# Kernel tuning notes

Measured on AMD Instinct MI355X. Metric: run time of the kernel, lower is better.

## Reference

```python
import jax, jax.numpy as jnp
import numpy as np

L, B, T, C, H, V = 12, 4, 1024, 768, 12, 50257
D = C // H
SCALE = 1.0 / float(np.sqrt(D))
EPS = 1e-5


def layernorm(x, g, b):
    m = jnp.mean(x, axis=-1, keepdims=True)
    v = jnp.var(x, axis=-1, keepdims=True)
    return (x - m) / jnp.sqrt(v + EPS) * g + b


def setup_inputs() -> dict:
    key = jax.random.key(0)
    ks = jax.random.split(key, 12)
    w = lambda k, shape: jax.random.normal(k, shape, jnp.float32) * 0.02
    return {
        "idx": jax.random.randint(ks[0], (B, T), 0, V),
        "tok_emb": w(ks[1], (V, C)),
        "pos_emb": w(ks[2], (1, T, C)),
        # per-layer stacked params (leading dim L); Linear stored [in, out]
        "wq": w(ks[3], (L, C, C)), "bq": jnp.zeros((L, C)),
        "wk": w(ks[4], (L, C, C)), "bk": jnp.zeros((L, C)),
        "wv": w(ks[5], (L, C, C)), "bv": jnp.zeros((L, C)),
        "wo": w(ks[6], (L, C, C)), "bo": jnp.zeros((L, C)),
        "ln1_g": jnp.ones((L, C)), "ln1_b": jnp.zeros((L, C)),
        "ln2_g": jnp.ones((L, C)), "ln2_b": jnp.zeros((L, C)),
        "w1": w(ks[7], (L, C, 4 * C)), "b1": jnp.zeros((L, 4 * C)),
        "w2": w(ks[8], (L, 4 * C, C)), "b2": jnp.zeros((L, C)),
        "lnf_g": jnp.ones((C,)), "lnf_b": jnp.zeros((C,)),
        "head_w": w(ks[9], (C, V)),
    }


def gpt_forward(idx, tok_emb, pos_emb, wq, bq, wk, bk, wv, bv, wo, bo,
                ln1_g, ln1_b, ln2_g, ln2_b, w1, b1, w2, b2,
                lnf_g, lnf_b, head_w):
    t = idx.shape[1]
    x = tok_emb[idx] + pos_emb[:, :t, :]                     # [B,T,C]
    mask = jnp.tril(jnp.ones((t, t), dtype=bool))            # causal

    def block(x, p):
        (pwq, pbq, pwk, pbk, pwv, pbv, pwo, pbo,
         g1, be1, g2, be2, pw1, pb1, pw2, pb2) = p
        h = layernorm(x, g1, be1)
        q = (h @ pwq + pbq).reshape(B, t, H, D)
        k = (h @ pwk + pbk).reshape(B, t, H, D)
        v = (h @ pwv + pbv).reshape(B, t, H, D)
        att = jnp.einsum('bthd,bshd->bhts', q, k) * SCALE    # [B,H,T,T]
        att = jnp.where(mask, att, -jnp.inf)
        att = jax.nn.softmax(att, axis=-1)
        y = jnp.einsum('bhts,bshd->bthd', att, v).reshape(B, t, C)
        x = x + y @ pwo + pbo
        h = layernorm(x, g2, be2)
        x = x + jax.nn.gelu(h @ pw1 + pb1, approximate=False) @ pw2 + pb2
        return x, None

    x, _ = jax.lax.scan(block, x, (wq, bq, wk, bk, wv, bv, wo, bo,
                                   ln1_g, ln1_b, ln2_g, ln2_b,
                                   w1, b1, w2, b2))
    x = layernorm(x, lnf_g, lnf_b)
    return x @ head_w                                        # logits [B,T,V]


def reference(idx, tok_emb, pos_emb, wq, bq, wk, bk, wv, bv, wo, bo,
              ln1_g, ln1_b, ln2_g, ln2_b, w1, b1, w2, b2,
              lnf_g, lnf_b, head_w):
    return gpt_forward(idx, tok_emb, pos_emb, wq, bq, wk, bk, wv, bv, wo, bo,
                       ln1_g, ln1_b, ln2_g, ln2_b, w1, b1, w2, b2,
                       lnf_g, lnf_b, head_w)
```

## Files before the change

kernel.cpp:

```cpp
#include <hip/hip_runtime.h>
#include <hip/hip_bf16.h>
#include <math.h>

#define L_ 12
#define B_ 4
#define T_ 1024
#define C_ 768
#define H_ 12
#define D_ 64
#define V_ 50257
#define M_ 4096
#define QKVN 2304
#define FF_ 3072
#define VPAD_ 51200

typedef __hip_bfloat16 bf16;
typedef __attribute__((ext_vector_type(4))) float f32x4;
typedef __attribute__((ext_vector_type(4))) short short4v;
typedef __attribute__((ext_vector_type(8))) short short8;
typedef __attribute__((ext_vector_type(8))) __bf16 bf16x8;

typedef __attribute__((address_space(1))) void gvoid;
typedef __attribute__((address_space(3))) void svoid;

__device__ __forceinline__ f32x4 mfma_bf16(short8 a, short8 b, f32x4 c) {
  return __builtin_amdgcn_mfma_f32_16x16x32_bf16(
      __builtin_bit_cast(bf16x8, a), __builtin_bit_cast(bf16x8, b), c, 0, 0, 0);
}

__device__ __forceinline__ void gload_lds16(const void* g, void* l) {
  __builtin_amdgcn_global_load_lds((gvoid*)(void*)g, (svoid*)l, 16, 0, 0);
}

__device__ __forceinline__ short f2bf(float x) {
  return __builtin_bit_cast(short, __float2bfloat16(x));
}

__global__ __launch_bounds__(256) void embed_kernel(const int* __restrict__ idx,
    const float* __restrict__ tok, const float* __restrict__ pos, float* __restrict__ x)
{
  const int row = blockIdx.x;
  const int t = row & (T_ - 1);
  const int id = idx[row];
  const float* te = tok + (size_t)id * C_;
  const float* pe = pos + (size_t)t * C_;
  float* xr = x + (size_t)row * C_;
  const int tid = threadIdx.x;
  xr[tid]       = te[tid]       + pe[tid];
  xr[tid + 256] = te[tid + 256] + pe[tid + 256];
  xr[tid + 512] = te[tid + 512] + pe[tid + 512];
}

__global__ __launch_bounds__(256) void ln_kernel(const float* __restrict__ x,
    const float* __restrict__ g, const float* __restrict__ be, bf16* __restrict__ out)
{
  const int w = threadIdx.x >> 6, l = threadIdx.x & 63;
  const int row = blockIdx.x * 4 + w;
  const float* xr = x + (size_t)row * C_;
  f32x4 v[3];
  float s = 0.0f, ss = 0.0f;
#pragma unroll
  for (int p = 0; p < 3; p++) {
    v[p] = *(const f32x4*)&xr[p * 256 + l * 4];
#pragma unroll
    for (int e = 0; e < 4; e++) { s += v[p][e]; ss += v[p][e] * v[p][e]; }
  }
#pragma unroll
  for (int o = 32; o >= 1; o >>= 1) { s += __shfl_xor(s, o, 64); ss += __shfl_xor(ss, o, 64); }
  const float mean = s * (1.0f / C_);
  const float rstd = rsqrtf(ss * (1.0f / C_) - mean * mean + 1e-5f);
  bf16* orow = out + (size_t)row * C_;
#pragma unroll
  for (int p = 0; p < 3; p++) {
    const f32x4 gg = *(const f32x4*)&g[p * 256 + l * 4];
    const f32x4 bb = *(const f32x4*)&be[p * 256 + l * 4];
    short4v o4;
#pragma unroll
    for (int e = 0; e < 4; e++) o4[e] = f2bf((v[p][e] - mean) * rstd * gg[e] + bb[e]);
    *(short4v*)&orow[p * 256 + l * 4] = o4;
  }
}

__global__ __launch_bounds__(256) void convt_kernel(const float* __restrict__ in,
    bf16* __restrict__ out, int K, int N, long in_ls, long out_ls, int row_off)
{
  __shared__ float tile[64][65];
  in  += (size_t)blockIdx.z * in_ls;
  out += (size_t)blockIdx.z * out_ls;
  const int k0 = blockIdx.x * 64, n0 = blockIdx.y * 64;
  const int tid = threadIdx.x;
#pragma unroll
  for (int ph = 0; ph < 4; ph++) {
    const int lk = ph * 16 + (tid >> 4);
    const int ln = (tid & 15) * 4;
    const int gn = n0 + ln;
    const float* src = &in[(size_t)(k0 + lk) * N + gn];
    f32x4 vv;
    if (gn + 4 <= N) {
      vv = *(const f32x4*)src;
    } else {
#pragma unroll
      for (int e = 0; e < 4; e++) vv[e] = (gn + e < N) ? src[e] : 0.0f;
    }
    *(f32x4*)&tile[lk][ln] = vv;
  }
  __syncthreads();
#pragma unroll
  for (int ph = 0; ph < 2; ph++) {
    const int lon = ph * 32 + (tid >> 3);
    const int lok0 = (tid & 7) * 8;
    short8 o;
#pragma unroll
    for (int e = 0; e < 8; e++) o[e] = f2bf(tile[lok0 + e][lon]);
    *(short8*)&out[(size_t)(row_off + n0 + lon) * K + k0 + lok0] = o;
  }
}

__global__ __launch_bounds__(256) void packb_kernel(const float* __restrict__ bq,
    const float* __restrict__ bk, const float* __restrict__ bv, float* __restrict__ out)
{
  const int i = blockIdx.x * 256 + threadIdx.x;
  const int ly = i / QKVN, c = i % QKVN;
  float v;
  if (c < C_)            v = bq[ly * C_ + c];
  else if (c < 2 * C_)   v = bk[ly * C_ + c - C_];
  else                   v = bv[ly * C_ + c - 2 * C_];
  out[i] = v;
}

template<bool BIAS, bool GELU, bool RESID, bool BF16OUT, bool VT>
__global__ __launch_bounds__(256) void gemm_bt(
    const short* __restrict__ A, const short* __restrict__ Bt,
    const float* __restrict__ bias, const float* resid,
    void* out, short* __restrict__ vt, int M, int N, int K)
{
  __shared__ short As[128 * 64];
  __shared__ short Bs[128 * 64];
  const int tid = threadIdx.x;
  const int w = tid >> 6, l = tid & 63;
  const int l15 = l & 15, l4 = l >> 4;
  const int wr = w >> 1, wc = w & 1;
  const int nwg = gridDim.x * gridDim.y;
  const int id = blockIdx.y * gridDim.x + blockIdx.x;
  const int chunk = nwg >> 3;
  const int swz = (id & 7) * chunk + (id >> 3);
  const long m0 = (long)(swz % gridDim.x) * 128;
  const long n0 = (long)(swz / gridDim.x) * 128;

  f32x4 acc[4][4] = {};
  const int lrow8 = l >> 3;
  const int lc = l & 7;

  for (int kt = 0; kt < K; kt += 64) {
#pragma unroll
    for (int j = 0; j < 8; j++) {
      const int c = w * 8 + j;
      const int isA = (c < 16);
      const int cc = isA ? c : (c - 16);
      const int row = cc * 8 + lrow8;
      const int colsw = ((lc ^ (row & 7)) << 3);
      const short* gp = (isA ? A + (size_t)(m0 + row) * K : Bt + (size_t)(n0 + row) * K) + kt + colsw;
      short* sp = (isA ? As : Bs) + row * 64 + (lc << 3);
      gload_lds16(gp, sp);
    }
    __syncthreads();
#pragma unroll
    for (int ks = 0; ks < 2; ks++) {
      short8 af[4], bfr[4];
#pragma unroll
      for (int i = 0; i < 4; i++) {
        int row = wr * 64 + i * 16 + l15;
        int cs = (ks * 32 + l4 * 8) ^ ((row & 7) << 3);
        af[i] = *(const short8*)&As[row * 64 + cs];
      }
#pragma unroll
      for (int jn = 0; jn < 4; jn++) {
        int row = wc * 64 + jn * 16 + l15;
        int cs = (ks * 32 + l4 * 8) ^ ((row & 7) << 3);
        bfr[jn] = *(const short8*)&Bs[row * 64 + cs];
      }
#pragma unroll
      for (int i = 0; i < 4; i++)
#pragma unroll
        for (int jn = 0; jn < 4; jn++)
          acc[i][jn] = mfma_bf16(af[i], bfr[jn], acc[i][jn]);
    }
    __syncthreads();
  }

#pragma unroll
  for (int i = 0; i < 4; i++) {
    const long rbase = m0 + wr * 64 + i * 16 + l4 * 4;
#pragma unroll
    for (int jn = 0; jn < 4; jn++) {
      const long col = n0 + wc * 64 + jn * 16 + l15;
      const float bv = BIAS ? bias[col] : 0.0f;
      if (VT && col >= 2 * C_) {
        const int hd = (int)col - 2 * C_;
        const int b = (int)(rbase >> 10);
        const int t0 = (int)(rbase & 1023);
        short4v o4;
#pragma unroll
        for (int r = 0; r < 4; r++) o4[r] = f2bf(acc[i][jn][r] + bv);
        *(short4v*)&vt[((size_t)(b * H_) * D_ + hd) * T_ + t0] = o4;
      } else {
#pragma unroll
        for (int r = 0; r < 4; r++) {
          float v = acc[i][jn][r] + bv;
          if (GELU) v = 0.5f * v * (1.0f + erff(v * 0.70710678118654752f));
          const size_t o = (size_t)(rbase + r) * (size_t)N + col;
          if (RESID)        ((float*)out)[o] = resid[o] + v;
          else if (BF16OUT) ((bf16*)out)[o] = __float2bfloat16(v);
          else              ((float*)out)[o] = v;
        }
      }
    }
  }
}

template<bool BIAS, bool GELU, bool RESID, bool BF16OUT>
__global__ __launch_bounds__(256) void gemm64(
    const short* __restrict__ A, const short* __restrict__ Bt,
    const float* __restrict__ bias, const float* resid,
    void* out, int M, int N, int K)
{
  __shared__ short As[64 * 64];
  __shared__ short Bs[128 * 64];
  const int tid = threadIdx.x;
  const int w = tid >> 6, l = tid & 63;
  const int l15 = l & 15, l4 = l >> 4;
  const int wm = w >> 1, wn = w & 1;
  const int nwg = gridDim.x * gridDim.y;
  const int id = blockIdx.y * gridDim.x + blockIdx.x;
  const int chunk = nwg >> 3;
  const int swz = (id & 7) * chunk + (id >> 3);
  const long m0 = (long)(swz % gridDim.x) * 64;
  const long n0 = (long)(swz / gridDim.x) * 128;
  const int rr = tid >> 3, g = tid & 7;

  f32x4 acc[2][4] = {};

  for (int kt = 0; kt < K; kt += 64) {
#pragma unroll
    for (int p = 0; p < 2; p++) {
      const int row = p * 32 + rr;
      const int cg = ((g ^ (row & 7)) << 3);
      gload_lds16(A + (size_t)(m0 + row) * K + kt + cg, &As[row * 64 + g * 8]);
    }
#pragma unroll
    for (int p = 0; p < 4; p++) {
      const int row = p * 32 + rr;
      const int cg = ((g ^ (row & 7)) << 3);
      gload_lds16(Bt + (size_t)(n0 + row) * K + kt + cg, &Bs[row * 64 + g * 8]);
    }
    __syncthreads();
#pragma unroll
    for (int ks = 0; ks < 2; ks++) {
      short8 af[2], bfr[4];
#pragma unroll
      for (int i = 0; i < 2; i++) {
        int row = wm * 32 + i * 16 + l15;
        int cs = (ks * 32 + l4 * 8) ^ ((row & 7) << 3);
        af[i] = *(const short8*)&As[row * 64 + cs];
      }
#pragma unroll
      for (int j = 0; j < 4; j++) {
        int row = wn * 64 + j * 16 + l15;
        int cs = (ks * 32 + l4 * 8) ^ ((row & 7) << 3);
        bfr[j] = *(const short8*)&Bs[row * 64 + cs];
      }
#pragma unroll
      for (int i = 0; i < 2; i++)
#pragma unroll
        for (int j = 0; j < 4; j++)
          acc[i][j] = mfma_bf16(af[i], bfr[j], acc[i][j]);
    }
    __syncthreads();
  }

#pragma unroll
  for (int i = 0; i < 2; i++) {
    const long rbase = m0 + wm * 32 + i * 16 + l4 * 4;
#pragma unroll
    for (int j = 0; j < 4; j++) {
      const long col = n0 + wn * 64 + j * 16 + l15;
      const float bv = BIAS ? bias[col] : 0.0f;
#pragma unroll
      for (int r = 0; r < 4; r++) {
        float v = acc[i][j][r] + bv;
        if (GELU) v = 0.5f * v * (1.0f + erff(v * 0.70710678118654752f));
        const size_t o = (size_t)(rbase + r) * (size_t)N + col;
        if (RESID)        ((float*)out)[o] = resid[o] + v;
        else if (BF16OUT) ((bf16*)out)[o] = __float2bfloat16(v);
        else              ((float*)out)[o] = v;
      }
    }
  }
}

__global__ __launch_bounds__(512, 1) void gemm256(
    const short* __restrict__ A, const short* __restrict__ Bt,
    float* __restrict__ out, int N, int K)
{
  __shared__ short As[2][256 * 64];
  __shared__ short Bs[2][256 * 64];
  const int tid = threadIdx.x;
  const int l = tid & 63, l15 = l & 15, l4 = l >> 4;
  const int wv = tid >> 6, wm = wv >> 2, wn = wv & 3;
  const int bid = blockIdx.x;
  const int x = bid & 7, r = bid >> 3;
  const int mt = (x & 1) * 8 + (r & 7);
  const int nt = (x >> 1) * 50 + (r >> 3);
  const long m0 = (long)mt * 256;
  const long n0 = (long)nt * 256;
  const int nkt = K >> 6;
  const int rr = tid >> 3, g = tid & 7;

  f32x4 acc[8][4] = {};

  auto stA = [&](int s, int kt, int off) {
#pragma unroll
    for (int p = 0; p < 2; p++) {
      const int row = p * 128 + off + rr;
      gload_lds16(A + (size_t)(m0 + row) * K + (kt << 6) + ((g ^ (row & 7)) << 3),
                  &As[s][row * 64 + g * 8]);
    }
  };
  auto stB = [&](int s, int kt, int off) {
#pragma unroll
    for (int p = 0; p < 2; p++) {
      const int row = p * 128 + ((rr >> 5) << 6) + (rr & 31) + off;
      gload_lds16(Bt + (size_t)(n0 + row) * K + (kt << 6) + ((g ^ (row & 7)) << 3),
                  &Bs[s][row * 64 + g * 8]);
    }
  };
  auto rdA = [&](int s, int mf, int ks) {
    const int row = wm * 128 + mf * 16 + l15;
    const int cs = (ks * 32 + l4 * 8) ^ ((row & 7) << 3);
    return *(const short8*)&As[s][row * 64 + cs];
  };
  auto rdB = [&](int s, int nf, int ks) {
    const int row = wn * 64 + nf * 16 + l15;
    const int cs = (ks * 32 + l4 * 8) ^ ((row & 7) << 3);
    return *(const short8*)&Bs[s][row * 64 + cs];
  };

  stA(0, 0, 0); stB(0, 0, 0); stA(0, 0, 64); stB(0, 0, 32);

  int q = 0;
  for (int kt = 0; kt < nkt; ++kt, q ^= 1) {
    const int ktn = (kt + 1 < nkt) ? kt + 1 : kt;
    short8 a0[2][4], a1[2][4], b0[2][2], b1[2][2];

    stA(q ^ 1, ktn, 0);
    asm volatile("s_waitcnt vmcnt(6)" ::: "memory");
    __builtin_amdgcn_s_barrier();
#pragma unroll
    for (int ks = 0; ks < 2; ks++) {
#pragma unroll
      for (int f = 0; f < 4; f++) a0[ks][f] = rdA(q, f, ks);
#pragma unroll
      for (int j = 0; j < 2; j++) b0[ks][j] = rdB(q, j, ks);
    }
    __builtin_amdgcn_s_setprio(1);
#pragma unroll
    for (int f = 0; f < 4; f++)
#pragma unroll
      for (int j = 0; j < 2; j++) {
        acc[f][j] = mfma_bf16(a0[0][f], b0[0][j], acc[f][j]);
        acc[f][j] = mfma_bf16(a0[1][f], b0[1][j], acc[f][j]);
      }
    __builtin_amdgcn_s_setprio(0);

    stB(q ^ 1, ktn, 0);
    asm volatile("s_waitcnt vmcnt(6)" ::: "memory");
    __builtin_amdgcn_s_barrier();
#pragma unroll
    for (int ks = 0; ks < 2; ks++)
#pragma unroll
      for (int f = 0; f < 4; f++) a1[ks][f] = rdA(q, f + 4, ks);
    __builtin_amdgcn_s_setprio(1);
#pragma unroll
    for (int f = 0; f < 4; f++)
#pragma unroll
      for (int j = 0; j < 2; j++) {
        acc[f + 4][j] = mfma_bf16(a1[0][f], b0[0][j], acc[f + 4][j]);
        acc[f + 4][j] = mfma_bf16(a1[1][f], b0[1][j], acc[f + 4][j]);
      }
    __builtin_amdgcn_s_setprio(0);

    stA(q ^ 1, ktn, 64);
    asm volatile("s_waitcnt vmcnt(6)" ::: "memory");
    __builtin_amdgcn_s_barrier();
#pragma unroll
    for (int ks = 0; ks < 2; ks++)
#pragma unroll
      for (int j = 0; j < 2; j++) b1[ks][j] = rdB(q, j + 2, ks);
    __builtin_amdgcn_s_setprio(1);
#pragma unroll
    for (int f = 0; f < 4; f++)
#pragma unroll
      for (int j = 0; j < 2; j++) {
        acc[f][j + 2] = mfma_bf16(a0[0][f], b1[0][j], acc[f][j + 2]);
        acc[f][j + 2] = mfma_bf16(a0[1][f], b1[1][j], acc[f][j + 2]);
      }
    __builtin_amdgcn_s_setprio(0);

    stB(q ^ 1, ktn, 32);
    __builtin_amdgcn_s_setprio(1);
#pragma unroll
    for (int f = 0; f < 4; f++)
#pragma unroll
      for (int j = 0; j < 2; j++) {
        acc[f + 4][j + 2] = mfma_bf16(a1[0][f], b1[0][j], acc[f + 4][j + 2]);
        acc[f + 4][j + 2] = mfma_bf16(a1[1][f], b1[1][j], acc[f + 4][j + 2]);
      }
    __builtin_amdgcn_s_setprio(0);
  }

#pragma unroll
  for (int i = 0; i < 8; i++) {
#pragma unroll
    for (int j = 0; j < 4; j++) {
      const long col = n0 + wn * 64 + j * 16 + l15;
      if (col >= N) continue;
#pragma unroll
      for (int r2 = 0; r2 < 4; r2++) {
        const long row = m0 + wm * 128 + i * 16 + l4 * 4 + r2;
        out[(size_t)row * (size_t)N + col] = acc[i][j][r2];
      }
    }
  }
}

__global__ __launch_bounds__(256) void attn_kernel(const short* __restrict__ qkv,
    const short* __restrict__ vt, bf16* __restrict__ y)
{
  __shared__ short Ks[2][64 * 64];
  __shared__ short Vs[2][64 * 64];
  const int qt = (gridDim.x - 1) - blockIdx.x;
  const int bh = blockIdx.y;
  const int b = bh / H_, h = bh % H_;
  const int tid = threadIdx.x, w = tid >> 6, l = tid & 63;
  const int l15 = l & 15, l4 = l >> 4;
  const int qrow0 = qt * 64 + w * 16;
  const float SC2 = 0.125f * 1.44269504088896f;

  auto stageKV = [&](int s, int s0) {
    const short* kbase = qkv + (size_t)(b * T_ + s0) * QKVN + C_ + h * D_;
    const short* vsrc = vt + (size_t)bh * D_ * T_ + s0;
#pragma unroll
    for (int ph = 0; ph < 2; ph++) {
      int r = ph * 32 + (tid >> 3);
      int gk = ((tid & 7) ^ ((r & 3) | (((r >> 3) & 1) << 2))) << 3;
      int gv = ((tid & 7) ^ (r & 7)) << 3;
      gload_lds16(kbase + (size_t)r * QKVN + gk, &Ks[s][r * 64 + (tid & 7) * 8]);
      gload_lds16(vsrc + (size_t)r * T_ + gv, &Vs[s][r * 64 + (tid & 7) * 8]);
    }
  };

  short8 qf[2];
#pragma unroll
  for (int kf = 0; kf < 2; kf++)
    qf[kf] = *(const short8*)&qkv[(size_t)(b * T_ + qrow0 + l15) * QKVN + h * D_ + kf * 32 + l4 * 8];

  f32x4 O[4] = {};
  float mst = -1e30f, lst = 0.0f;

  stageKV(0, 0);
  __syncthreads();

  int cur = 0;
  const int qg = qrow0 + l15;
  const int send = qt * 64 + 64;
  for (int s0 = 0; s0 < send; s0 += 64) {
    if (s0 + 64 < send) stageKV(cur ^ 1, s0 + 64);
    f32x4 S[4];
#pragma unroll
    for (int c = 0; c < 4; c++) {
      const int row = 8 * (l15 >> 2) + (l15 & 3) + 4 * (c & 1) + 32 * (c >> 1);
      const int swz = (row & 3) | (((row >> 3) & 1) << 2);
      short8 k0 = *(const short8*)&Ks[cur][row * 64 + ((l4 ^ swz) << 3)];
      short8 k1 = *(const short8*)&Ks[cur][row * 64 + (((4 + l4) ^ swz) << 3)];
      f32x4 z = {0.0f, 0.0f, 0.0f, 0.0f};
      z = mfma_bf16(k0, qf[0], z);
      z = mfma_bf16(k1, qf[1], z);
      S[c] = z;
    }
#pragma unroll
    for (int c = 0; c < 4; c++) {
      const int kvb = s0 + 8 * l4 + 4 * (c & 1) + 32 * (c >> 1);
#pragma unroll
      for (int r = 0; r < 4; r++) {
        const float v = S[c][r] * SC2;
        S[c][r] = (kvb + r <= qg) ? v : -1e30f;
      }
    }
    float pm = -1e30f;
#pragma unroll
    for (int c = 0; c < 4; c++)
#pragma unroll
      for (int r = 0; r < 4; r++) pm = fmaxf(pm, S[c][r]);
    float mn;
    if (__all(pm - mst <= 8.0f)) {
      mn = mst;
    } else {
      float pm2 = fmaxf(pm, __shfl_xor(pm, 16, 64));
      pm2 = fmaxf(pm2, __shfl_xor(pm2, 32, 64));
      mn = fmaxf(mst, pm2);
      const float al = exp2f(mst - mn);
      mst = mn;
      lst *= al;
#pragma unroll
      for (int r = 0; r < 4; r++) {
        const float alr = __shfl(al, l4 * 4 + r, 16);
#pragma unroll
        for (int df = 0; df < 4; df++) O[df][r] *= alr;
      }
    }
    float rs = 0.0f;
    float pvv[4][4];
#pragma unroll
    for (int c = 0; c < 4; c++)
#pragma unroll
      for (int r = 0; r < 4; r++) { pvv[c][r] = exp2f(S[c][r] - mn); rs += pvv[c][r]; }
    rs += __shfl_xor(rs, 16, 64);
    rs += __shfl_xor(rs, 32, 64);
    lst += rs;
    short8 pa[2];
#pragma unroll
    for (int ks = 0; ks < 2; ks++)
#pragma unroll
      for (int r = 0; r < 4; r++) {
        pa[ks][r]     = f2bf(pvv[2 * ks][r]);
        pa[ks][r + 4] = f2bf(pvv[2 * ks + 1][r]);
      }
#pragma unroll
    for (int df = 0; df < 4; df++) {
      const int row = df * 16 + l15;
      short8 v0 = *(const short8*)&Vs[cur][row * 64 + ((l4 ^ (row & 7)) << 3)];
      short8 v1 = *(const short8*)&Vs[cur][row * 64 + ((((4 + l4)) ^ (row & 7)) << 3)];
      O[df] = mfma_bf16(pa[0], v0, O[df]);
      O[df] = mfma_bf16(pa[1], v1, O[df]);
    }
    __syncthreads();
    cur ^= 1;
  }

  const float inv = 1.0f / lst;
#pragma unroll
  for (int r = 0; r < 4; r++) {
    const float invr = __shfl(inv, l4 * 4 + r, 16);
    const size_t row = (size_t)(b * T_ + qrow0 + l4 * 4 + r);
#pragma unroll
    for (int df = 0; df < 4; df++)
      y[row * C_ + h * D_ + df * 16 + l15] = __float2bfloat16(O[df][r] * invr);
  }
}

extern "C" void kernel_launch(void* const* d_in, const int* in_sizes, int n_in,
                              void* d_out, int out_size, void* d_ws, size_t ws_size,
                              hipStream_t stream)
{
  const int*   idx  = (const int*)d_in[0];
  const float* tok  = (const float*)d_in[1];
  const float* pos  = (const float*)d_in[2];
  const float* wq   = (const float*)d_in[3];
  const float* bq   = (const float*)d_in[4];
  const float* wk   = (const float*)d_in[5];
  const float* bk   = (const float*)d_in[6];
  const float* wv   = (const float*)d_in[7];
  const float* bv   = (const float*)d_in[8];
  const float* wo   = (const float*)d_in[9];
  const float* bo   = (const float*)d_in[10];
  const float* ln1g = (const float*)d_in[11];
  const float* ln1b = (const float*)d_in[12];
  const float* ln2g = (const float*)d_in[13];
  const float* ln2b = (const float*)d_in[14];
  const float* w1   = (const float*)d_in[15];
  const float* b1   = (const float*)d_in[16];
  const float* w2   = (const float*)d_in[17];
  const float* b2   = (const float*)d_in[18];
  const float* lnfg = (const float*)d_in[19];
  const float* lnfb = (const float*)d_in[20];
  const float* headw= (const float*)d_in[21];

  char* p = (char*)d_ws;
  size_t off = 0;
  auto alloc = [&](size_t n) { void* r = p + off; off += (n + 255) & ~(size_t)255; return r; };
  short* qkvT  = (short*)alloc((size_t)L_ * QKVN * C_ * 2);
  short* woT   = (short*)alloc((size_t)L_ * C_ * C_ * 2);
  short* w1T   = (short*)alloc((size_t)L_ * FF_ * C_ * 2);
  short* w2T   = (short*)alloc((size_t)L_ * C_ * FF_ * 2);
  short* headT = (short*)alloc((size_t)VPAD_ * C_ * 2);
  float* qkvb  = (float*)alloc((size_t)L_ * QKVN * 4);
  float* x     = (float*)alloc((size_t)M_ * C_ * 4);
  bf16*  h     = (bf16*)alloc((size_t)M_ * C_ * 2);
  short* qkvB  = (short*)alloc((size_t)M_ * QKVN * 2);
  short* vt    = (short*)alloc((size_t)B_ * H_ * D_ * T_ * 2);
  short* y     = (short*)alloc((size_t)M_ * C_ * 2);
  short* hid   = (short*)alloc((size_t)M_ * FF_ * 2);
  if (off > ws_size) return;

  convt_kernel<<<dim3(12, 12, 12), 256, 0, stream>>>(wq, (bf16*)qkvT, C_, C_, (long)C_ * C_, (long)QKVN * C_, 0);
  convt_kernel<<<dim3(12, 12, 12), 256, 0, stream>>>(wk, (bf16*)qkvT, C_, C_, (long)C_ * C_, (long)QKVN * C_, C_);
  convt_kernel<<<dim3(12, 12, 12), 256, 0, stream>>>(wv, (bf16*)qkvT, C_, C_, (long)C_ * C_, (long)QKVN * C_, 2 * C_);
  convt_kernel<<<dim3(12, 12, 12), 256, 0, stream>>>(wo, (bf16*)woT, C_, C_, (long)C_ * C_, (long)C_ * C_, 0);
  convt_kernel<<<dim3(12, 48, 12), 256, 0, stream>>>(w1, (bf16*)w1T, C_, FF_, (long)C_ * FF_, (long)FF_ * C_, 0);
  convt_kernel<<<dim3(48, 12, 12), 256, 0, stream>>>(w2, (bf16*)w2T, FF_, C_, (long)FF_ * C_, (long)C_ * FF_, 0);
  convt_kernel<<<dim3(12, VPAD_ / 64, 1), 256, 0, stream>>>(headw, (bf16*)headT, C_, V_, 0, 0, 0);
  packb_kernel<<<dim3(108), 256, 0, stream>>>(bq, bk, bv, qkvb);

  embed_kernel<<<dim3(M_), 256, 0, stream>>>(idx, tok, pos, x);

  for (int ly = 0; ly < L_; ly++) {
    ln_kernel<<<dim3(M_ / 4), 256, 0, stream>>>(x, ln1g + ly * C_, ln1b + ly * C_, h);
    gemm_bt<true, false, false, true, true><<<dim3(32, 18), 256, 0, stream>>>(
        (const short*)h, qkvT + (size_t)ly * QKVN * C_, qkvb + ly * QKVN, nullptr, qkvB, vt, M_, QKVN, C_);
    attn_kernel<<<dim3(16, 48), 256, 0, stream>>>(qkvB, vt, (bf16*)y);
    gemm64<true, false, true, false><<<dim3(64, 6), 256, 0, stream>>>(
        y, woT + (size_t)ly * C_ * C_, bo + ly * C_, x, x, M_, C_, C_);
    ln_kernel<<<dim3(M_ / 4), 256, 0, stream>>>(x, ln2g + ly * C_, ln2b + ly * C_, h);
    gemm_bt<true, true, false, true, false><<<dim3(32, 24), 256, 0, stream>>>(
        (const short*)h, w1T + (size_t)ly * FF_ * C_, b1 + ly * FF_, nullptr, hid, nullptr, M_, FF_, C_);
    gemm64<true, false, true, false><<<dim3(64, 6), 256, 0, stream>>>(
        hid, w2T + (size_t)ly * C_ * FF_, b2 + ly * C_, x, x, M_, C_, FF_);
  }

  ln_kernel<<<dim3(M_ / 4), 256, 0, stream>>>(x, lnfg, lnfb, h);
  gemm256<<<dim3(3200), 512, 0, stream>>>((const short*)h, headT, (float*)d_out, V_, C_);
}
```

Baseline: 3.040 ms.

## Double-buffer gemm_bt, replace head GEMM with 128-tile kernel, tweak attention

Adds LDS double buffering to gemm_bt so the next K tile loads while MFMAs run on the current one. Replaces the 256x256 LM-head GEMM with a 128x128 double-buffered kernel at two blocks per CU, and shrinks the vocab padding to 50688. The attention kernel skips causal masking on fully-visible key blocks and raises wave priority around its MFMA sections. These changes trade the head kernel's finer-grained pipelining for smaller tiles and less padded work, and double gemm_bt's LDS use, which may reduce occupancy.

```diff
diff --git a/kernel.cpp b/kernel.cpp
--- a/kernel.cpp
+++ b/kernel.cpp
@@ -12,7 +12,7 @@
 #define M_ 4096
 #define QKVN 2304
 #define FF_ 3072
-#define VPAD_ 51200
+#define VPAD_ 50688
 
 typedef __hip_bfloat16 bf16;
 typedef __attribute__((ext_vector_type(4))) float f32x4;
@@ -134,8 +134,8 @@
     const float* __restrict__ bias, const float* resid,
     void* out, short* __restrict__ vt, int M, int N, int K)
 {
-  __shared__ short As[128 * 64];
-  __shared__ short Bs[128 * 64];
+  __shared__ short As[2][128 * 64];
+  __shared__ short Bs[2][128 * 64];
   const int tid = threadIdx.x;
   const int w = tid >> 6, l = tid & 63;
   const int l15 = l & 15, l4 = l >> 4;
@@ -146,12 +146,13 @@
   const int swz = (id & 7) * chunk + (id >> 3);
   const long m0 = (long)(swz % gridDim.x) * 128;
   const long n0 = (long)(swz / gridDim.x) * 128;
-
-  f32x4 acc[4][4] = {};
+  const int nkt = K >> 6;
   const int lrow8 = l >> 3;
   const int lc = l & 7;
 
-  for (int kt = 0; kt < K; kt += 64) {
+  f32x4 acc[4][4] = {};
+
+  auto stage = [&](int s, int kt) {
 #pragma unroll
     for (int j = 0; j < 8; j++) {
       const int c = w * 8 + j;
@@ -159,11 +160,18 @@
       const int cc = isA ? c : (c - 16);
       const int row = cc * 8 + lrow8;
       const int colsw = ((lc ^ (row & 7)) << 3);
-      const short* gp = (isA ? A + (size_t)(m0 + row) * K : Bt + (size_t)(n0 + row) * K) + kt + colsw;
-      short* sp = (isA ? As : Bs) + row * 64 + (lc << 3);
+      const short* gp = (isA ? A + (size_t)(m0 + row) * K : Bt + (size_t)(n0 + row) * K) + (kt << 6) + colsw;
+      short* sp = (isA ? As[s] : Bs[s]) + row * 64 + (lc << 3);
       gload_lds16(gp, sp);
     }
-    __syncthreads();
+  };
+
+  stage(0, 0);
+  int q = 0;
+  for (int kt = 0; kt < nkt; ++kt, q ^= 1) {
+    asm volatile("s_waitcnt vmcnt(0)" ::: "memory");
+    __builtin_amdgcn_s_barrier();
+    if (kt + 1 < nkt) stage(q ^ 1, kt + 1);
 #pragma unroll
     for (int ks = 0; ks < 2; ks++) {
       short8 af[4], bfr[4];
@@ -171,13 +179,13 @@
       for (int i = 0; i < 4; i++) {
         int row = wr * 64 + i * 16 + l15;
         int cs = (ks * 32 + l4 * 8) ^ ((row & 7) << 3);
-        af[i] = *(const short8*)&As[row * 64 + cs];
+        af[i] = *(const short8*)&As[q][row * 64 + cs];
       }
 #pragma unroll
       for (int jn = 0; jn < 4; jn++) {
         int row = wc * 64 + jn * 16 + l15;
         int cs = (ks * 32 + l4 * 8) ^ ((row & 7) << 3);
-        bfr[jn] = *(const short8*)&Bs[row * 64 + cs];
+        bfr[jn] = *(const short8*)&Bs[q][row * 64 + cs];
       }
 #pragma unroll
       for (int i = 0; i < 4; i++)
@@ -185,7 +193,6 @@
         for (int jn = 0; jn < 4; jn++)
           acc[i][jn] = mfma_bf16(af[i], bfr[jn], acc[i][jn]);
     }
-    __syncthreads();
   }
 
 #pragma unroll
@@ -298,137 +305,81 @@
   }
 }
 
-__global__ __launch_bounds__(512, 1) void gemm256(
+__global__ __launch_bounds__(256, 2) void gemm128h(
     const short* __restrict__ A, const short* __restrict__ Bt,
     float* __restrict__ out, int N, int K)
 {
-  __shared__ short As[2][256 * 64];
-  __shared__ short Bs[2][256 * 64];
+  __shared__ short As[2][128 * 64];
+  __shared__ short Bs[2][128 * 64];
   const int tid = threadIdx.x;
-  const int l = tid & 63, l15 = l & 15, l4 = l >> 4;
-  const int wv = tid >> 6, wm = wv >> 2, wn = wv & 3;
+  const int w = tid >> 6, l = tid & 63;
+  const int l15 = l & 15, l4 = l >> 4;
+  const int wr = w >> 1, wc = w & 1;
   const int bid = blockIdx.x;
   const int x = bid & 7, r = bid >> 3;
-  const int mt = (x & 1) * 8 + (r & 7);
-  const int nt = (x >> 1) * 50 + (r >> 3);
-  const long m0 = (long)mt * 256;
-  const long n0 = (long)nt * 256;
+  const int mt = (x & 1) * 16 + (r & 15);
+  const int nt = (x >> 1) * 99 + (r >> 4);
+  const long m0 = (long)mt * 128;
+  const long n0 = (long)nt * 128;
   const int nkt = K >> 6;
-  const int rr = tid >> 3, g = tid & 7;
-
-  f32x4 acc[8][4] = {};
-
-  auto stA = [&](int s, int kt, int off) {
-#pragma unroll
-    for (int p = 0; p < 2; p++) {
-      const int row = p * 128 + off + rr;
-      gload_lds16(A + (size_t)(m0 + row) * K + (kt << 6) + ((g ^ (row & 7)) << 3),
-                  &As[s][row * 64 + g * 8]);
+  const int lrow8 = l >> 3;
+  const int lc = l & 7;
+
+  f32x4 acc[4][4] = {};
+
+  auto stage = [&](int s, int kt) {
+#pragma unroll
+    for (int j = 0; j < 8; j++) {
+      const int c = w * 8 + j;
+      const int isA = (c < 16);
+      const int cc = isA ? c : (c - 16);
+      const int row = cc * 8 + lrow8;
+      const int colsw = ((lc ^ (row & 7)) << 3);
+      const short* gp = (isA ? A + (size_t)(m0 + row) * K : Bt + (size_t)(n0 + row) * K) + (kt << 6) + colsw;
+      short* sp = (isA ? As[s] : Bs[s]) + row * 64 + (lc << 3);
+      gload_lds16(gp, sp);
     }
   };
-  auto stB = [&](int s, int kt, int off) {
-#pragma unroll
-    for (int p = 0; p < 2; p++) {
-      const int row = p * 128 + ((rr >> 5) << 6) + (rr & 31) + off;
-      gload_lds16(Bt + (size_t)(n0 + row) * K + (kt << 6) + ((g ^ (row & 7)) << 3),
-                  &Bs[s][row * 64 + g * 8]);
-    }
-  };
-  auto rdA = [&](int s, int mf, int ks) {
-    const int row = wm * 128 + mf * 16 + l15;
-    const int cs = (ks * 32 + l4 * 8) ^ ((row & 7) << 3);
-    return *(const short8*)&As[s][row * 64 + cs];
-  };
-  auto rdB = [&](int s, int nf, int ks) {
-    const int row = wn * 64 + nf * 16 + l15;
-    const int cs = (ks * 32 + l4 * 8) ^ ((row & 7) << 3);
-    return *(const short8*)&Bs[s][row * 64 + cs];
-  };
-
-  stA(0, 0, 0); stB(0, 0, 0); stA(0, 0, 64); stB(0, 0, 32);
-
+
+  stage(0, 0);
   int q = 0;
   for (int kt = 0; kt < nkt; ++kt, q ^= 1) {
-    const int ktn = (kt + 1 < nkt) ? kt + 1 : kt;
-    short8 a0[2][4], a1[2][4], b0[2][2], b1[2][2];
-
-    stA(q ^ 1, ktn, 0);
-    asm volatile("s_waitcnt vmcnt(6)" ::: "memory");
+    asm volatile("s_waitcnt vmcnt(0)" ::: "memory");
     __builtin_amdgcn_s_barrier();
+    if (kt + 1 < nkt) stage(q ^ 1, kt + 1);
 #pragma unroll
     for (int ks = 0; ks < 2; ks++) {
-#pragma unroll
-      for (int f = 0; f < 4; f++) a0[ks][f] = rdA(q, f, ks);
-#pragma unroll
-      for (int j = 0; j < 2; j++) b0[ks][j] = rdB(q, j, ks);
-    }
-    __builtin_amdgcn_s_setprio(1);
-#pragma unroll
-    for (int f = 0; f < 4; f++)
-#pragma unroll
-      for (int j = 0; j < 2; j++) {
-        acc[f][j] = mfma_bf16(a0[0][f], b0[0][j], acc[f][j]);
-        acc[f][j] = mfma_bf16(a0[1][f], b0[1][j], acc[f][j]);
-      }
-    __builtin_amdgcn_s_setprio(0);
-
-    stB(q ^ 1, ktn, 0);
-    asm volatile("s_waitcnt vmcnt(6)" ::: "memory");
-    __builtin_amdgcn_s_barrier();
-#pragma unroll
-    for (int ks = 0; ks < 2; ks++)
-#pragma unroll
-      for (int f = 0; f < 4; f++) a1[ks][f] = rdA(q, f + 4, ks);
-    __builtin_amdgcn_s_setprio(1);
-#pragma unroll
-    for (int f = 0; f < 4; f++)
-#pragma unroll
-      for (int j = 0; j < 2; j++) {
-        acc[f + 4][j] = mfma_bf16(a1[0][f], b0[0][j], acc[f + 4][j]);
-        acc[f + 4][j] = mfma_bf16(a1[1][f], b0[1][j], acc[f + 4][j]);
-      }
-    __builtin_amdgcn_s_setprio(0);
-
-    stA(q ^ 1, ktn, 64);
-    asm volatile("s_waitcnt vmcnt(6)" ::: "memory");
-    __builtin_amdgcn_s_barrier();
-#pragma unroll
-    for (int ks = 0; ks < 2; ks++)
-#pragma unroll
-      for (int j = 0; j < 2; j++) b1[ks][j] = rdB(q, j + 2, ks);
-    __builtin_amdgcn_s_setprio(1);
-#pragma unroll
-    for (int f = 0; f < 4; f++)
-#pragma unroll
-      for (int j = 0; j < 2; j++) {
-        acc[f][j + 2] = mfma_bf16(a0[0][f], b1[0][j], acc[f][j + 2]);
-        acc[f][j + 2] = mfma_bf16(a0[1][f], b1[1][j], acc[f][j + 2]);
-      }
-    __builtin_amdgcn_s_setprio(0);
-
-    stB(q ^ 1, ktn, 32);
-    __builtin_amdgcn_s_setprio(1);
-#pragma unroll
-    for (int f = 0; f < 4; f++)
-#pragma unroll
-      for (int j = 0; j < 2; j++) {
-        acc[f + 4][j + 2] = mfma_bf16(a1[0][f], b1[0][j], acc[f + 4][j + 2]);
-        acc[f + 4][j + 2] = mfma_bf16(a1[1][f], b1[1][j], acc[f + 4][j + 2]);
-      }
-    __builtin_amdgcn_s_setprio(0);
-  }
-
-#pragma unroll
-  for (int i = 0; i < 8; i++) {
-#pragma unroll
-    for (int j = 0; j < 4; j++) {
-      const long col = n0 + wn * 64 + j * 16 + l15;
+      short8 af[4], bfr[4];
+#pragma unroll
+      for (int i = 0; i < 4; i++) {
+        int row = wr * 64 + i * 16 + l15;
+        int cs = (ks * 32 + l4 * 8) ^ ((row & 7) << 3);
+        af[i] = *(const short8*)&As[q][row * 64 + cs];
+      }
+#pragma unroll
+      for (int jn = 0; jn < 4; jn++) {
+        int row = wc * 64 + jn * 16 + l15;
+        int cs = (ks * 32 + l4 * 8) ^ ((row & 7) << 3);
+        bfr[jn] = *(const short8*)&Bs[q][row * 64 + cs];
+      }
+#pragma unroll
+      for (int i = 0; i < 4; i++)
+#pragma unroll
+        for (int jn = 0; jn < 4; jn++)
+          acc[i][jn] = mfma_bf16(af[i], bfr[jn], acc[i][jn]);
+    }
+  }
+
+#pragma unroll
+  for (int i = 0; i < 4; i++) {
+    const long rbase = m0 + wr * 64 + i * 16 + l4 * 4;
+#pragma unroll
+    for (int jn = 0; jn < 4; jn++) {
+      const long col = n0 + wc * 64 + jn * 16 + l15;
       if (col >= N) continue;
 #pragma unroll
-      for (int r2 = 0; r2 < 4; r2++) {
-        const long row = m0 + wm * 128 + i * 16 + l4 * 4 + r2;
-        out[(size_t)row * (size_t)N + col] = acc[i][j][r2];
-      }
+      for (int r2 = 0; r2 < 4; r2++)
+        out[(size_t)(rbase + r2) * (size_t)N + col] = acc[i][jn][r2];
     }
   }
 }
@@ -476,6 +427,7 @@
   for (int s0 = 0; s0 < send; s0 += 64) {
     if (s0 + 64 < send) stageKV(cur ^ 1, s0 + 64);
     f32x4 S[4];
+    __builtin_amdgcn_s_setprio(1);
 #pragma unroll
     for (int c = 0; c < 4; c++) {
       const int row = 8 * (l15 >> 2) + (l15 & 3) + 4 * (c & 1) + 32 * (c >> 1);
@@ -487,13 +439,21 @@
       z = mfma_bf16(k1, qf[1], z);
       S[c] = z;
     }
-#pragma unroll
-    for (int c = 0; c < 4; c++) {
-      const int kvb = s0 + 8 * l4 + 4 * (c & 1) + 32 * (c >> 1);
-#pragma unroll
-      for (int r = 0; r < 4; r++) {
-        const float v = S[c][r] * SC2;
-        S[c][r] = (kvb + r <= qg) ? v : -1e30f;
+    __builtin_amdgcn_s_setprio(0);
+    if (s0 + 63 <= qrow0) {
+#pragma unroll
+      for (int c = 0; c < 4; c++)
+#pragma unroll
+        for (int r = 0; r < 4; r++) S[c][r] *= SC2;
+    } else {
+#pragma unroll
+      for (int c = 0; c < 4; c++) {
+        const int kvb = s0 + 8 * l4 + 4 * (c & 1) + 32 * (c >> 1);
+#pragma unroll
+        for (int r = 0; r < 4; r++) {
+          const float v = S[c][r] * SC2;
+          S[c][r] = (kvb + r <= qg) ? v : -1e30f;
+        }
       }
     }
     float pm = -1e30f;
@@ -535,6 +495,7 @@
         pa[ks][r]     = f2bf(pvv[2 * ks][r]);
         pa[ks][r + 4] = f2bf(pvv[2 * ks + 1][r]);
       }
+    __builtin_amdgcn_s_setprio(1);
 #pragma unroll
     for (int df = 0; df < 4; df++) {
       const int row = df * 16 + l15;
@@ -543,6 +504,7 @@
       O[df] = mfma_bf16(pa[0], v0, O[df]);
       O[df] = mfma_bf16(pa[1], v1, O[df]);
     }
+    __builtin_amdgcn_s_setprio(0);
     __syncthreads();
     cur ^= 1;
   }
@@ -628,5 +590,5 @@
   }
 
   ln_kernel<<<dim3(M_ / 4), 256, 0, stream>>>(x, lnfg, lnfb, h);
-  gemm256<<<dim3(3200), 512, 0, stream>>>((const short*)h, headT, (float*)d_out, V_, C_);
-}
+  gemm128h<<<dim3(32 * (VPAD_ / 128)), 256, 0, stream>>>((const short*)h, headT, (float*)d_out, V_, C_);
+}
```

Result: slower. 3.267 ms (+7.5%).
